# Kernel tuning notes

Measured on AMD Instinct MI355X. Metric: run time of the kernel, lower is better.

The kernel has to match this reference:

```python
import jax, jax.numpy as jnp
import numpy as np

BZ, QL, KL, D = 8, 2048, 2048, 128
SCALE = 1.0 / (D ** 0.5)
NEG = -1000000000.0


def setup_inputs() -> dict:
    key = jax.random.key(0)
    kq, kk, kv, km = jax.random.split(key, 4)
    q = jax.random.normal(kq, (BZ, QL, D), dtype=jnp.float32)
    k = jax.random.normal(kk, (BZ, KL, D), dtype=jnp.float32)
    v = jax.random.normal(kv, (BZ, KL, D), dtype=jnp.float32)
    mask = jax.random.randint(km, (BZ, KL), 0, 2).astype(jnp.bool_)
    return {"q": q, "k": k, "v": v, "mask": mask}


def reference(q, k, v, mask):
    # scores: (bz, q_len, k_len)
    score = jnp.einsum('bqd,bkd->bqk', q, k) * SCALE
    # masked_fill where ~mask (padding positions) with -1e9
    score = jnp.where(mask[:, None, :], score, NEG)
    weights = jax.nn.softmax(score, axis=-1)
    # (bz, q_len, v_dim)
    return jnp.einsum('bqk,bkd->bqd', weights, v)
```

## Files before the change

### kernel.cpp

```cpp
#include <hip/hip_runtime.h>
#include <hip/hip_bf16.h>


#define BZ 8
#define QL 2048
#define KLEN 2048
#define DH 128
#define NSL 64
#define SLICE_E 4096
#define PPITCH 40

typedef float f32x4 __attribute__((ext_vector_type(4)));
typedef int   i32x4 __attribute__((ext_vector_type(4)));
typedef __bf16 bf16x8 __attribute__((ext_vector_type(8)));
typedef __bf16 bf16x4 __attribute__((ext_vector_type(4)));
typedef __bf16 bf16x2 __attribute__((ext_vector_type(2)));

#define QSC 0.12751879523298232f
#define NEGV -1000000000.0f

__global__ void prep_kv(const float* __restrict__ kg, const float* __restrict__ vg,
                        __bf16* __restrict__ khat, __bf16* __restrict__ vhat) {
  const int blk = blockIdx.x;
  const int bs = blk & 511;
  const int b = bs >> 6, s = bs & 63;
  const int tid = threadIdx.x;
#pragma unroll
  for (int i = 0; i < 2; ++i) {
    const int c = i * 256 + tid;
    const int ln = c & 63, lc = ln & 15, qd = ln >> 4;
    if (blk < 512) {
      const int ff = (c >> 6) & 1, kf = c >> 7;
      const int key = s * 32 + ff * 16 + lc;
      const float* src = kg + ((size_t)(b * KLEN + key)) * DH + kf * 32 + qd * 8;
      f32x4 a = *(const f32x4*)src;
      f32x4 d = *(const f32x4*)(src + 4);
      bf16x8 w;
      w[0]=(__bf16)a[0]; w[1]=(__bf16)a[1]; w[2]=(__bf16)a[2]; w[3]=(__bf16)a[3];
      w[4]=(__bf16)d[0]; w[5]=(__bf16)d[1]; w[6]=(__bf16)d[2]; w[7]=(__bf16)d[3];
      *(bf16x8*)&khat[((size_t)bs * 512 + c) * 8] = w;
    } else {
      const int nt = c >> 6;
      const float* src = vg + ((size_t)(b * KLEN + s * 32 + qd * 8)) * DH + nt * 16 + lc;
      bf16x8 w;
#pragma unroll
      for (int j = 0; j < 8; ++j) w[j] = (__bf16)src[(size_t)j * DH];
      *(bf16x8*)&vhat[((size_t)bs * 512 + c) * 8] = w;
    }
  }
}

__global__ __launch_bounds__(512, 2) void fattn7(
    const __bf16* __restrict__ khat, const __bf16* __restrict__ vhat,
    const float* __restrict__ qg_, const int* __restrict__ maskg,
    float* __restrict__ outg) {
  __shared__ __align__(16) __bf16 sP[8][2][16 * PPITCH];
  __shared__ __align__(16) float fb[8192 + 64];

  const int tid = threadIdx.x;
  const int wv = tid >> 6, ln = tid & 63;
  const int qd = ln >> 4, lc = ln & 15;
  const int ab = blockIdx.x & 7, qt = blockIdx.x >> 3;
  const int q0 = qt * 64;
  const int qg = wv & 1, sl = wv >> 1;

  bf16x8 qf[2][4];
#pragma unroll
  for (int qp = 0; qp < 2; ++qp) {
    const float* qr = qg_ + ((size_t)(ab * QL + q0 + qg * 32 + qp * 16 + lc)) * DH + qd * 8;
#pragma unroll
    for (int kf = 0; kf < 4; ++kf) {
      f32x4 a = *(const f32x4*)(qr + kf * 32);
      f32x4 c = *(const f32x4*)(qr + kf * 32 + 4);
      bf16x8 t;
      t[0]=(__bf16)(a[0]*QSC); t[1]=(__bf16)(a[1]*QSC); t[2]=(__bf16)(a[2]*QSC); t[3]=(__bf16)(a[3]*QSC);
      t[4]=(__bf16)(c[0]*QSC); t[5]=(__bf16)(c[1]*QSC); t[6]=(__bf16)(c[2]*QSC); t[7]=(__bf16)(c[3]*QSC);
      qf[qp][kf] = t;
    }
  }

  const __bf16* Kb = khat + (size_t)ab * NSL * SLICE_E;
  const __bf16* Vb = vhat + (size_t)ab * NSL * SLICE_E;
  const int* mrow = maskg + ab * KLEN;
  __bf16* sp0 = &sP[wv][0][0];
  __bf16* sp1 = &sP[wv][1][0];

  f32x4 oacc[2][8];
#pragma unroll
  for (int qp = 0; qp < 2; ++qp)
#pragma unroll
    for (int i = 0; i < 8; ++i) oacc[qp][i] = (f32x4){0.f, 0.f, 0.f, 0.f};
  float li[2] = {0.f, 0.f};

  bf16x8 kA[4][2], kN[4][2], vA[8];
  {
    const __bf16* ks = Kb + (size_t)(sl * 16) * SLICE_E;
#pragma unroll
    for (int kf = 0; kf < 4; ++kf)
#pragma unroll
      for (int f = 0; f < 2; ++f)
        kA[kf][f] = *(const bf16x8*)&ks[((kf * 2 + f) * 64 + ln) * 8];
  }
  i32x4 mc0 = *(const i32x4*)&mrow[sl * 16 * 32 + qd * 4];
  i32x4 mc1 = *(const i32x4*)&mrow[sl * 16 * 32 + 16 + qd * 4];

  for (int it = 0; it < 16; ++it) {
    const int s = sl * 16 + it;
    const __bf16* vs = Vb + (size_t)s * SLICE_E;

#pragma unroll
    for (int nt = 0; nt < 8; ++nt)
      vA[nt] = *(const bf16x8*)&vs[(nt * 64 + ln) * 8];

    const int sn = (it < 15) ? s + 1 : s;
    const __bf16* ksn = Kb + (size_t)sn * SLICE_E;
#pragma unroll
    for (int kf = 0; kf < 4; ++kf)
#pragma unroll
      for (int f = 0; f < 2; ++f)
        kN[kf][f] = *(const bf16x8*)&ksn[((kf * 2 + f) * 64 + ln) * 8];
    i32x4 mn0 = *(const i32x4*)&mrow[sn * 32 + qd * 4];
    i32x4 mn1 = *(const i32x4*)&mrow[sn * 32 + 16 + qd * 4];

    f32x4 sa[2][2];
#pragma unroll
    for (int f = 0; f < 2; ++f)
#pragma unroll
      for (int qp = 0; qp < 2; ++qp) sa[f][qp] = (f32x4){0.f, 0.f, 0.f, 0.f};
#pragma unroll
    for (int kf = 0; kf < 4; ++kf)
#pragma unroll
      for (int f = 0; f < 2; ++f) {
        sa[f][0] = __builtin_amdgcn_mfma_f32_16x16x32_bf16(kA[kf][f], qf[0][kf], sa[f][0], 0, 0, 0);
        sa[f][1] = __builtin_amdgcn_mfma_f32_16x16x32_bf16(kA[kf][f], qf[1][kf], sa[f][1], 0, 0, 0);
      }

#pragma unroll
    for (int qp = 0; qp < 2; ++qp) {
      float ps[2][4];
#pragma unroll
      for (int r = 0; r < 4; ++r) {
        float p0 = __builtin_amdgcn_exp2f(sa[0][qp][r]);
        float p1 = __builtin_amdgcn_exp2f(sa[1][qp][r]);
        ps[0][r] = mc0[r] ? p0 : 0.f;
        ps[1][r] = mc1[r] ? p1 : 0.f;
      }
      li[qp] += ((ps[0][0] + ps[0][1]) + (ps[0][2] + ps[0][3])) +
                ((ps[1][0] + ps[1][1]) + (ps[1][2] + ps[1][3]));
      __bf16* sp = (qp == 0) ? sp0 : sp1;
#pragma unroll
      for (int f = 0; f < 2; ++f) {
        bf16x4 pw;
        pw[0] = (__bf16)ps[f][0]; pw[1] = (__bf16)ps[f][1];
        pw[2] = (__bf16)ps[f][2]; pw[3] = (__bf16)ps[f][3];
        *(bf16x4*)&sp[lc * PPITCH + f * 16 + qd * 4] = pw;
      }
    }
    bf16x8 pf0 = *(const bf16x8*)&sp0[lc * PPITCH + qd * 8];
    bf16x8 pf1 = *(const bf16x8*)&sp1[lc * PPITCH + qd * 8];

#pragma unroll
    for (int nt = 0; nt < 8; ++nt) {
      oacc[0][nt] = __builtin_amdgcn_mfma_f32_16x16x32_bf16(vA[nt], pf0, oacc[0][nt], 0, 0, 0);
      oacc[1][nt] = __builtin_amdgcn_mfma_f32_16x16x32_bf16(vA[nt], pf1, oacc[1][nt], 0, 0, 0);
    }

#pragma unroll
    for (int kf = 0; kf < 4; ++kf)
#pragma unroll
      for (int f = 0; f < 2; ++f) kA[kf][f] = kN[kf][f];
    mc0 = mn0; mc1 = mn1;
  }

#pragma unroll
  for (int qp = 0; qp < 2; ++qp) {
    li[qp] += __shfl_xor(li[qp], 16, 64);
    li[qp] += __shfl_xor(li[qp], 32, 64);
  }

  f32x4* mOv = (f32x4*)fb;
  float* sml = fb + 8192;
  auto publish = [&]() {
#pragma unroll
    for (int qp = 0; qp < 2; ++qp) {
#pragma unroll
      for (int nt = 0; nt < 8; ++nt)
        mOv[((qg * 2 + qp) * 8 + nt) * 64 + ln] = oacc[qp][nt];
      if (qd == 0) sml[(qg * 2 + qp) * 16 + lc] = li[qp];
    }
  };
  auto absorb = [&]() {
#pragma unroll
    for (int qp = 0; qp < 2; ++qp) {
      li[qp] += sml[(qg * 2 + qp) * 16 + lc];
#pragma unroll
      for (int nt = 0; nt < 8; ++nt) {
        f32x4 o2 = mOv[((qg * 2 + qp) * 8 + nt) * 64 + ln];
#pragma unroll
        for (int r = 0; r < 4; ++r) oacc[qp][nt][r] += o2[r];
      }
    }
  };

  __syncthreads();
  if (sl == 3) publish();
  __syncthreads();
  if (sl == 2) absorb();
  __syncthreads();
  if (sl == 1) publish();
  __syncthreads();
  if (sl == 0) absorb();
  __syncthreads();
  if (sl == 2) publish();
  __syncthreads();
  if (sl == 0) {
    absorb();
#pragma unroll
    for (int qp = 0; qp < 2; ++qp) {
      const float invL = 1.0f / li[qp];
      float* orow = outg + ((size_t)(ab * QL + q0 + qg * 32 + qp * 16 + lc)) * DH;
#pragma unroll
      for (int nt = 0; nt < 8; ++nt) {
        f32x4 res;
#pragma unroll
        for (int r = 0; r < 4; ++r) res[r] = oacc[qp][nt][r] * invL;
        *(f32x4*)&orow[nt * 16 + qd * 4] = res;
      }
    }
  }
}

#define KT 64
#define KPITCH 136
#define VPITCH 72
#define PPITCH2 72

__global__ __launch_bounds__(256, 1) void fattn_mono(
    const float* __restrict__ qgp, const float* __restrict__ kg,
    const float* __restrict__ vg, const int* __restrict__ maskg,
    float* __restrict__ outg) {
  __shared__ __bf16 sK[KT][KPITCH];
  __shared__ __bf16 sVT[DH][VPITCH];
  __shared__ __bf16 sPm[4][16][PPITCH2];

  const int tid = threadIdx.x;
  const int wv = tid >> 6, ln = tid & 63;
  const int qd = ln >> 4, lc = ln & 15;
  const int bid = blockIdx.x;
  const int b = bid >> 5;
  const int q0 = (bid & 31) << 6;
  const int qw = q0 + (wv << 4);

  bf16x8 qf[4];
  {
    const float* qr = qgp + ((size_t)(b * QL + qw + lc)) * DH + qd * 8;
#pragma unroll
    for (int kf = 0; kf < 4; ++kf) {
      f32x4 a = *(const f32x4*)(qr + kf * 32);
      f32x4 c = *(const f32x4*)(qr + kf * 32 + 4);
      bf16x8 t;
      t[0]=(__bf16)(a[0]*QSC); t[1]=(__bf16)(a[1]*QSC); t[2]=(__bf16)(a[2]*QSC); t[3]=(__bf16)(a[3]*QSC);
      t[4]=(__bf16)(c[0]*QSC); t[5]=(__bf16)(c[1]*QSC); t[6]=(__bf16)(c[2]*QSC); t[7]=(__bf16)(c[3]*QSC);
      qf[kf] = t;
    }
  }

  const float* kb = kg + (size_t)b * KLEN * DH;
  const float* vb = vg + (size_t)b * KLEN * DH;
  const int* mrow = maskg + b * KLEN;

  f32x4 kreg[8], va[4], vbr[4];

  auto load_tile = [&](int t) {
    const float* kt = kb + ((size_t)t * KT) * DH;
#pragma unroll
    for (int it = 0; it < 8; ++it) {
      int f = it * 256 + tid;
      kreg[it] = *(const f32x4*)(kt + (size_t)(f >> 5) * DH + (f & 31) * 4);
    }
    const float* vt = vb + ((size_t)t * KT) * DH;
#pragma unroll
    for (int it = 0; it < 4; ++it) {
      int u = it * 256 + tid;
      int m = u & 31, dc = (u >> 5) * 4;
      va[it]  = *(const f32x4*)(vt + (size_t)(2 * m) * DH + dc);
      vbr[it] = *(const f32x4*)(vt + (size_t)(2 * m + 1) * DH + dc);
    }
  };
  auto store_tile = [&]() {
#pragma unroll
    for (int it = 0; it < 8; ++it) {
      int f = it * 256 + tid;
      bf16x4 w;
      w[0]=(__bf16)kreg[it][0]; w[1]=(__bf16)kreg[it][1];
      w[2]=(__bf16)kreg[it][2]; w[3]=(__bf16)kreg[it][3];
      *(bf16x4*)&sK[f >> 5][(f & 31) * 4] = w;
    }
#pragma unroll
    for (int it = 0; it < 4; ++it) {
      int u = it * 256 + tid;
      int m = u & 31, dc = (u >> 5) * 4;
#pragma unroll
      for (int j = 0; j < 4; ++j) {
        bf16x2 p2;
        p2[0] = (__bf16)va[it][j];
        p2[1] = (__bf16)vbr[it][j];
        *(bf16x2*)&sVT[dc + j][2 * m] = p2;
      }
    }
  };

  f32x4 oacc[8];
#pragma unroll
  for (int i = 0; i < 8; ++i) oacc[i] = (f32x4){0.f, 0.f, 0.f, 0.f};
  float mi[4] = {-INFINITY, -INFINITY, -INFINITY, -INFINITY};
  float li[4] = {0.f, 0.f, 0.f, 0.f};

  load_tile(0); store_tile(); __syncthreads();

  for (int t = 0; t < (KLEN / KT); ++t) {
    const bool more = (t + 1 < (KLEN / KT));
    if (more) load_tile(t + 1);

    f32x4 sa[4];
#pragma unroll
    for (int f = 0; f < 4; ++f) sa[f] = (f32x4){0.f, 0.f, 0.f, 0.f};
#pragma unroll
    for (int kf = 0; kf < 4; ++kf)
#pragma unroll
      for (int f = 0; f < 4; ++f) {
        bf16x8 bk = *(const bf16x8*)&sK[f * 16 + lc][kf * 32 + qd * 8];
        sa[f] = __builtin_amdgcn_mfma_f32_16x16x32_bf16(qf[kf], bk, sa[f], 0, 0, 0);
      }

    const int kv0 = t * KT;
#pragma unroll
    for (int f = 0; f < 4; ++f) {
      const bool keep = mrow[kv0 + f * 16 + lc] != 0;
#pragma unroll
      for (int r = 0; r < 4; ++r) sa[f][r] = keep ? sa[f][r] : NEGV;
    }

    float rm[4], alpha[4], rs[4];
#pragma unroll
    for (int r = 0; r < 4; ++r)
      rm[r] = fmaxf(fmaxf(sa[0][r], sa[1][r]), fmaxf(sa[2][r], sa[3][r]));
#pragma unroll
    for (int sh = 0; sh < 4; ++sh) {
      const int off = 1 << sh;
#pragma unroll
      for (int r = 0; r < 4; ++r) rm[r] = fmaxf(rm[r], __shfl_xor(rm[r], off, 64));
    }
#pragma unroll
    for (int r = 0; r < 4; ++r) {
      float mn = fmaxf(mi[r], rm[r]);
      alpha[r] = __builtin_amdgcn_exp2f(mi[r] - mn);
      mi[r] = mn; rs[r] = 0.f;
    }
#pragma unroll
    for (int f = 0; f < 4; ++f)
#pragma unroll
      for (int r = 0; r < 4; ++r) {
        float p = __builtin_amdgcn_exp2f(sa[f][r] - mi[r]);
        sa[f][r] = p; rs[r] += p;
      }
#pragma unroll
    for (int sh = 0; sh < 4; ++sh) {
      const int off = 1 << sh;
#pragma unroll
      for (int r = 0; r < 4; ++r) rs[r] += __shfl_xor(rs[r], off, 64);
    }
#pragma unroll
    for (int r = 0; r < 4; ++r) li[r] = li[r] * alpha[r] + rs[r];

#pragma unroll
    for (int f = 0; f < 4; ++f)
#pragma unroll
      for (int r = 0; r < 4; ++r)
        sPm[wv][qd * 4 + r][f * 16 + lc] = (__bf16)sa[f][r];
#pragma unroll
    for (int nt = 0; nt < 8; ++nt)
#pragma unroll
      for (int r = 0; r < 4; ++r) oacc[nt][r] *= alpha[r];

#pragma unroll
    for (int kp = 0; kp < 2; ++kp) {
      bf16x8 ap = *(const bf16x8*)&sPm[wv][lc][kp * 32 + qd * 8];
#pragma unroll
      for (int nt = 0; nt < 8; ++nt) {
        bf16x8 bv = *(const bf16x8*)&sVT[nt * 16 + lc][kp * 32 + qd * 8];
        oacc[nt] = __builtin_amdgcn_mfma_f32_16x16x32_bf16(ap, bv, oacc[nt], 0, 0, 0);
      }
    }

    __syncthreads();
    if (more) store_tile();
    __syncthreads();
  }

  float inv[4];
#pragma unroll
  for (int r = 0; r < 4; ++r) inv[r] = 1.0f / li[r];
  float* orow = outg + ((size_t)(b * QL + qw)) * DH;
#pragma unroll
  for (int nt = 0; nt < 8; ++nt)
#pragma unroll
    for (int r = 0; r < 4; ++r)
      orow[(size_t)(qd * 4 + r) * DH + nt * 16 + lc] = oacc[nt][r] * inv[r];
}

extern "C" void kernel_launch(void* const* d_in, const int* in_sizes, int n_in,
                              void* d_out, int out_size, void* d_ws, size_t ws_size,
                              hipStream_t stream) {
  (void)in_sizes; (void)n_in; (void)out_size;
  const float* q = (const float*)d_in[0];
  const float* k = (const float*)d_in[1];
  const float* v = (const float*)d_in[2];
  const int* mask = (const int*)d_in[3];
  float* out = (float*)d_out;

  const size_t kv_elems = (size_t)BZ * KLEN * DH;
  if (ws_size >= 2 * kv_elems * sizeof(__bf16)) {
    __bf16* khat = (__bf16*)d_ws;
    __bf16* vhat = khat + kv_elems;
    prep_kv<<<dim3(1024), dim3(256), 0, stream>>>(k, v, khat, vhat);
    fattn7<<<dim3(256), dim3(512), 0, stream>>>(khat, vhat, q, mask, out);
  } else {
    fattn_mono<<<dim3(BZ * (QL / 64)), dim3(256), 0, stream>>>(q, k, v, mask, out);
  }
}
```

Baseline: 119.6 us.

## Software-pipeline attention loop so QK of next slice overlaps PV of previous

```diff
diff --git a/kernel.cpp b/kernel.cpp
--- a/kernel.cpp
+++ b/kernel.cpp
@@ -50,7 +50,7 @@
   }
 }
 
-__global__ __launch_bounds__(512, 2) void fattn7(
+__global__ __launch_bounds__(512, 2) void fattn8(
     const __bf16* __restrict__ khat, const __bf16* __restrict__ vhat,
     const float* __restrict__ qg_, const int* __restrict__ maskg,
     float* __restrict__ outg) {
@@ -92,49 +92,51 @@
     for (int i = 0; i < 8; ++i) oacc[qp][i] = (f32x4){0.f, 0.f, 0.f, 0.f};
   float li[2] = {0.f, 0.f};
 
-  bf16x8 kA[4][2], kN[4][2], vA[8];
-  {
-    const __bf16* ks = Kb + (size_t)(sl * 16) * SLICE_E;
+  bf16x8 kA[4][2], kB[4][2], vA[8];
+  bf16x8 pf0, pf1;
+  i32x4 mA0, mA1, mB0, mB1;
+  f32x4 sa[2][2];
+  const int s0 = sl * 16;
+
+  auto loadK = [&](bf16x8 (&dst)[4][2], int sidx) {
+    const __bf16* ks = Kb + (size_t)sidx * SLICE_E;
 #pragma unroll
     for (int kf = 0; kf < 4; ++kf)
 #pragma unroll
       for (int f = 0; f < 2; ++f)
-        kA[kf][f] = *(const bf16x8*)&ks[((kf * 2 + f) * 64 + ln) * 8];
-  }
-  i32x4 mc0 = *(const i32x4*)&mrow[sl * 16 * 32 + qd * 4];
-  i32x4 mc1 = *(const i32x4*)&mrow[sl * 16 * 32 + 16 + qd * 4];
-
-  for (int it = 0; it < 16; ++it) {
-    const int s = sl * 16 + it;
-    const __bf16* vs = Vb + (size_t)s * SLICE_E;
-
+        dst[kf][f] = *(const bf16x8*)&ks[((kf * 2 + f) * 64 + ln) * 8];
+  };
+  auto loadM = [&](i32x4& m0, i32x4& m1, int sidx) {
+    m0 = *(const i32x4*)&mrow[sidx * 32 + qd * 4];
+    m1 = *(const i32x4*)&mrow[sidx * 32 + 16 + qd * 4];
+  };
+  auto loadV = [&](int sidx) {
+    const __bf16* vs = Vb + (size_t)sidx * SLICE_E;
 #pragma unroll
     for (int nt = 0; nt < 8; ++nt)
       vA[nt] = *(const bf16x8*)&vs[(nt * 64 + ln) * 8];
-
-    const int sn = (it < 15) ? s + 1 : s;
-    const __bf16* ksn = Kb + (size_t)sn * SLICE_E;
+  };
+  auto qk = [&](const bf16x8 (&kk)[4][2]) {
+#pragma unroll
+    for (int f = 0; f < 2; ++f)
+#pragma unroll
+      for (int qp = 0; qp < 2; ++qp) sa[f][qp] = (f32x4){0.f, 0.f, 0.f, 0.f};
 #pragma unroll
     for (int kf = 0; kf < 4; ++kf)
 #pragma unroll
-      for (int f = 0; f < 2; ++f)
-        kN[kf][f] = *(const bf16x8*)&ksn[((kf * 2 + f) * 64 + ln) * 8];
-    i32x4 mn0 = *(const i32x4*)&mrow[sn * 32 + qd * 4];
-    i32x4 mn1 = *(const i32x4*)&mrow[sn * 32 + 16 + qd * 4];
-
-    f32x4 sa[2][2];
-#pragma unroll
-    for (int f = 0; f < 2; ++f)
-#pragma unroll
-      for (int qp = 0; qp < 2; ++qp) sa[f][qp] = (f32x4){0.f, 0.f, 0.f, 0.f};
-#pragma unroll
-    for (int kf = 0; kf < 4; ++kf)
-#pragma unroll
       for (int f = 0; f < 2; ++f) {
-        sa[f][0] = __builtin_amdgcn_mfma_f32_16x16x32_bf16(kA[kf][f], qf[0][kf], sa[f][0], 0, 0, 0);
-        sa[f][1] = __builtin_amdgcn_mfma_f32_16x16x32_bf16(kA[kf][f], qf[1][kf], sa[f][1], 0, 0, 0);
-      }
-
+        sa[f][0] = __builtin_amdgcn_mfma_f32_16x16x32_bf16(kk[kf][f], qf[0][kf], sa[f][0], 0, 0, 0);
+        sa[f][1] = __builtin_amdgcn_mfma_f32_16x16x32_bf16(kk[kf][f], qf[1][kf], sa[f][1], 0, 0, 0);
+      }
+  };
+  auto pv = [&]() {
+#pragma unroll
+    for (int nt = 0; nt < 8; ++nt) {
+      oacc[0][nt] = __builtin_amdgcn_mfma_f32_16x16x32_bf16(vA[nt], pf0, oacc[0][nt], 0, 0, 0);
+      oacc[1][nt] = __builtin_amdgcn_mfma_f32_16x16x32_bf16(vA[nt], pf1, oacc[1][nt], 0, 0, 0);
+    }
+  };
+  auto softmax = [&](const i32x4& m0, const i32x4& m1) {
 #pragma unroll
     for (int qp = 0; qp < 2; ++qp) {
       float ps[2][4];
@@ -142,8 +144,8 @@
       for (int r = 0; r < 4; ++r) {
         float p0 = __builtin_amdgcn_exp2f(sa[0][qp][r]);
         float p1 = __builtin_amdgcn_exp2f(sa[1][qp][r]);
-        ps[0][r] = mc0[r] ? p0 : 0.f;
-        ps[1][r] = mc1[r] ? p1 : 0.f;
+        ps[0][r] = m0[r] ? p0 : 0.f;
+        ps[1][r] = m1[r] ? p1 : 0.f;
       }
       li[qp] += ((ps[0][0] + ps[0][1]) + (ps[0][2] + ps[0][3])) +
                 ((ps[1][0] + ps[1][1]) + (ps[1][2] + ps[1][3]));
@@ -156,21 +158,46 @@
         *(bf16x4*)&sp[lc * PPITCH + f * 16 + qd * 4] = pw;
       }
     }
-    bf16x8 pf0 = *(const bf16x8*)&sp0[lc * PPITCH + qd * 8];
-    bf16x8 pf1 = *(const bf16x8*)&sp1[lc * PPITCH + qd * 8];
-
-#pragma unroll
-    for (int nt = 0; nt < 8; ++nt) {
-      oacc[0][nt] = __builtin_amdgcn_mfma_f32_16x16x32_bf16(vA[nt], pf0, oacc[0][nt], 0, 0, 0);
-      oacc[1][nt] = __builtin_amdgcn_mfma_f32_16x16x32_bf16(vA[nt], pf1, oacc[1][nt], 0, 0, 0);
-    }
-
-#pragma unroll
-    for (int kf = 0; kf < 4; ++kf)
-#pragma unroll
-      for (int f = 0; f < 2; ++f) kA[kf][f] = kN[kf][f];
-    mc0 = mn0; mc1 = mn1;
-  }
+    pf0 = *(const bf16x8*)&sp0[lc * PPITCH + qd * 8];
+    pf1 = *(const bf16x8*)&sp1[lc * PPITCH + qd * 8];
+  };
+
+  loadK(kA, s0);
+  loadM(mA0, mA1, s0);
+  loadK(kB, s0 + 1);
+  loadM(mB0, mB1, s0 + 1);
+  loadV(s0);
+  qk(kA);
+  softmax(mA0, mA1);
+
+  for (int du = 0; du < 7; ++du) {
+    {
+      const int it = 2 * du + 1, s = s0 + it;
+      loadK(kA, s + 1);
+      loadM(mA0, mA1, s + 1);
+      qk(kB);
+      pv();
+      loadV(s);
+      softmax(mB0, mB1);
+    }
+    {
+      const int it = 2 * du + 2, s = s0 + it;
+      loadK(kB, s + 1);
+      loadM(mB0, mB1, s + 1);
+      qk(kA);
+      pv();
+      loadV(s);
+      softmax(mA0, mA1);
+    }
+  }
+  {
+    const int s = s0 + 15;
+    qk(kB);
+    pv();
+    loadV(s);
+    softmax(mB0, mB1);
+  }
+  pv();
 
 #pragma unroll
   for (int qp = 0; qp < 2; ++qp) {
@@ -424,7 +451,7 @@
     __bf16* khat = (__bf16*)d_ws;
     __bf16* vhat = khat + kv_elems;
     prep_kv<<<dim3(1024), dim3(256), 0, stream>>>(k, v, khat, vhat);
-    fattn7<<<dim3(256), dim3(512), 0, stream>>>(khat, vhat, q, mask, out);
+    fattn8<<<dim3(256), dim3(512), 0, stream>>>(khat, vhat, q, mask, out);
   } else {
     fattn_mono<<<dim3(BZ * (QL / 64)), dim3(256), 0, stream>>>(q, k, v, mask, out);
   }
```

New measurement: 104.6 us. 12.5% less time.
